# Kernel optimization log

Hardware: AMD Instinct MI355X
Metric: run time of the kernel (lower is better)

## Reference

```python
import jax, jax.numpy as jnp
import numpy as np

EPS_GEN = 1e-7   # GENConv message epsilon
LN_EPS = 1e-5    # torch LayerNorm default eps


def _ln(x, g, b):
    mu = x.mean(-1, keepdims=True)
    v = ((x - mu) ** 2).mean(-1, keepdims=True)
    return (x - mu) / jnp.sqrt(v + LN_EPS) * g + b


def _genconv(x, src, dst, N, t, W1, b1, g1, be1, W2, b2):
    # GENConv(aggr='softmax', learn_t, num_layers=2, norm='layer'), no edge_attr
    msg = jax.nn.relu(x[src]) + EPS_GEN                 # [E,H] gather + eps
    z = msg * t
    m = jax.ops.segment_max(z, dst, num_segments=N)      # scatter-max [N,H]
    e = jnp.exp(z - m[dst])
    denom = jax.ops.segment_sum(e, dst, num_segments=N) + 1e-16
    alpha = e / denom[dst]                               # per-neighborhood softmax
    out = jax.ops.segment_sum(msg * alpha, dst, num_segments=N) + x  # aggregate + root
    h = jax.nn.relu(_ln(out @ W1 + b1, g1, be1))         # MLP [H,2H] + LN + ReLU
    return h @ W2 + b2                                   # [2H,H] plain last layer


def setup_inputs():
    key = jax.random.key(0)
    ks = jax.random.split(key, 24)
    N, E, Fin, H = 100000, 1600000, 16, 64
    s = 0.02
    d = {
        'x': jax.random.normal(ks[0], (N, Fin), jnp.float32),
        'edge_index': jax.random.randint(ks[1], (2, E), 0, N, dtype=jnp.int32),
        'W_enc': jax.random.normal(ks[2], (Fin, H), jnp.float32) * s,
        'b_enc': jnp.zeros((H,), jnp.float32),
        't1': jnp.float32(1.0),
        'W1a': jax.random.normal(ks[3], (H, 2 * H), jnp.float32) * s,
        'b1a': jnp.zeros((2 * H,), jnp.float32),
        'g1a': jnp.ones((2 * H,), jnp.float32),
        'be1a': jnp.zeros((2 * H,), jnp.float32),
        'W1b': jax.random.normal(ks[4], (2 * H, H), jnp.float32) * s,
        'b1b': jnp.zeros((H,), jnp.float32),
        'g_n1': jnp.ones((H,), jnp.float32),
        'b_n1': jnp.zeros((H,), jnp.float32),
        't2': jnp.float32(1.0),
        'W2a': jax.random.normal(ks[5], (H, 2 * H), jnp.float32) * s,
        'b2a': jnp.zeros((2 * H,), jnp.float32),
        'g2a': jnp.ones((2 * H,), jnp.float32),
        'be2a': jnp.zeros((2 * H,), jnp.float32),
        'W2b': jax.random.normal(ks[6], (2 * H, H), jnp.float32) * s,
        'b2b': jnp.zeros((H,), jnp.float32),
        'g_n0': jnp.ones((H,), jnp.float32),
        'b_n0': jnp.zeros((H,), jnp.float32),
        'W_lin': jax.random.normal(ks[7], (H, 1), jnp.float32) * s,
        'b_lin': jnp.zeros((1,), jnp.float32),
    }
    return d


def reference(x, edge_index, W_enc, b_enc, t1, W1a, b1a, g1a, be1a, W1b, b1b,
              g_n1, b_n1, t2, W2a, b2a, g2a, be2a, W2b, b2b, g_n0, b_n0,
              W_lin, b_lin):
    N = x.shape[0]
    src, dst = edge_index[0], edge_index[1]
    h = x @ W_enc + b_enc                                   # node encoder
    h = _genconv(h, src, dst, N, t1, W1a, b1a, g1a, be1a, W1b, b1b)  # layers[0].conv (bare)
    # layers[1]: DeepGCNLayer res+ -> x + conv(act(norm(x)))  (dropout = identity, deterministic ref)
    r = _genconv(jax.nn.relu(_ln(h, g_n1, b_n1)), src, dst, N, t2,
                 W2a, b2a, g2a, be2a, W2b, b2b)
    h = h + r
    h = jax.nn.relu(_ln(h, g_n0, b_n0))                     # layers[0].norm / act at the end
    logits = h @ W_lin + b_lin                              # [N,1]
    return jax.nn.sigmoid(logits), logits
```

## Files before the change

kernel.cpp:

```cpp
#include <hip/hip_runtime.h>
#include <math.h>

constexpr int HD   = 64;
constexpr int HD2  = 128;
constexpr int SCAP = 48;
constexpr int NPW  = 4;
constexpr int NPB  = 16;
constexpr int PSH  = 14;
constexpr int EPB  = 2048;

constexpr int SO = 68;
constexpr int SU = 132;
constexpr int SY = 68;

constexpr float FXS  = 8192.f;
constexpr float FXSI = 1.f / 8192.f;

typedef short  bf16x8 __attribute__((ext_vector_type(8)));
typedef float  f32x4  __attribute__((ext_vector_type(4)));

__device__ __forceinline__ unsigned short fix16(float v) {
    int q = (int)(fmaxf(v, 0.f) * FXS + 0.5f);
    return (unsigned short)min(q, 65535);
}

__device__ __forceinline__ float wave_sum(float v) {
#pragma unroll
    for (int off = 32; off > 0; off >>= 1) v += __shfl_xor(v, off, 64);
    return v;
}

__device__ __forceinline__ void splitf(float f, short& hi, short& lo) {
    unsigned u = __float_as_uint(f);
    hi = (short)(u >> 16);
    float lf = f - __uint_as_float(u & 0xffff0000u);
    lo = (short)(__float_as_uint(lf) >> 16);
}

__device__ __forceinline__ void split8(const float* p, bf16x8& hi, bf16x8& lo) {
    float v[8];
    *(float4*)&v[0] = *(const float4*)p;
    *(float4*)&v[4] = *(const float4*)(p + 4);
#pragma unroll
    for (int j = 0; j < 8; j++) { short h, l; splitf(v[j], h, l); hi[j] = h; lo[j] = l; }
}

__global__ void prep_kernel(const int* __restrict__ ei,
                            int* __restrict__ cursor, int* __restrict__ slots,
                            const float* __restrict__ x,
                            const float* __restrict__ W,
                            const float* __restrict__ b,
                            float* __restrict__ h,
                            unsigned short* __restrict__ g,
                            const float* __restrict__ L1W1, const float* __restrict__ L1W2,
                            const float* __restrict__ L2W1, const float* __restrict__ L2W2,
                            short* __restrict__ swz,
                            int E, int N, int SB, int encB) {
    if (blockIdx.x < (unsigned)SB) {
        int p = blockIdx.x & 7;
        int base = (blockIdx.x >> 3) * EPB;
        for (int off = threadIdx.x; off < EPB; off += 256) {
            int e = base + off;
            if (e < E) {
                int dst = ei[E + e];
                if ((dst >> PSH) == p) {
                    int src = ei[e];
                    int pos = atomicAdd(&cursor[dst], 1);
                    if (pos < SCAP) slots[(unsigned)(dst * SCAP + pos)] = src;
                }
            }
        }
    } else if (blockIdx.x < (unsigned)(SB + encB)) {
        int i = (blockIdx.x - SB) * 256 + threadIdx.x;
        if (i >= N * HD) return;
        int n = i >> 6, j = i & 63;
        const float* xr = x + (unsigned)(n * 16);
        float acc = b[j];
#pragma unroll
        for (int k = 0; k < 16; k++) acc += xr[k] * W[k * HD + j];
        h[i] = acc;
        g[i] = fix16(acc);
    } else {
        int sb = blockIdx.x - SB - encB;
        int layer = sb >> 3;
        int idx = (sb & 7) * 256 + threadIdx.x;
        const float* Wa = layer ? L2W1 : L1W1;
        const float* Wb = layer ? L2W2 : L1W2;
        short* base = swz + layer * 32768;
        if (idx < 1024) {
            int ks = idx >> 9, rem = idx & 511;
            int nt = rem >> 6, lane = rem & 63;
#pragma unroll
            for (int j = 0; j < 8; j++) {
                int k = ks * 32 + (lane >> 4) * 8 + j;
                int n = nt * 16 + (lane & 15);
                short hh, ll; splitf(Wa[k * HD2 + n], hh, ll);
                base[idx * 8 + j] = hh; base[8192 + idx * 8 + j] = ll;
            }
        } else {
            int jdx = idx - 1024;
            int ks = jdx >> 8, rem = jdx & 255;
            int nt = rem >> 6, lane = rem & 63;
#pragma unroll
            for (int j = 0; j < 8; j++) {
                int k = ks * 32 + (lane >> 4) * 8 + j;
                int n = nt * 16 + (lane & 15);
                short hh, ll; splitf(Wb[k * HD + n], hh, ll);
                base[16384 + jdx * 8 + j] = hh; base[24576 + jdx * 8 + j] = ll;
            }
        }
    }
}

template <int MODE>
__global__ void __launch_bounds__(256) conv_kernel(
    const unsigned short* __restrict__ gin,
    const float* __restrict__ hroot,
    const int* __restrict__ deg_arr, const int* __restrict__ slots,
    const float* __restrict__ tptr,
    const short* __restrict__ W1hi, const short* __restrict__ W1lo,
    const float* __restrict__ b1,
    const float* __restrict__ g1, const float* __restrict__ be1,
    const short* __restrict__ W2hi, const short* __restrict__ W2lo,
    const float* __restrict__ b2,
    const float* __restrict__ gn, const float* __restrict__ bn,
    const float* __restrict__ resid,
    const float* __restrict__ wlin, const float* __restrict__ blin,
    float* __restrict__ outA, unsigned short* __restrict__ outG, int N) {
    __shared__ float s_out[NPB][SO];
    __shared__ float s_u[NPB][SU];
    __shared__ float s_y[NPB][SY];
    int wv = threadIdx.x >> 6, j = threadIdx.x & 63;
    int q = j >> 4;
    int c = (j & 15) << 2;
    int nb = blockIdx.x * NPB + wv * NPW;
    float t = tptr[0];

    int deg[NPW], sid[NPW];
#pragma unroll
    for (int u = 0; u < NPW; u++) {
        int n = nb + u;
        int d = (n < N) ? min(deg_arr[n], SCAP) : 0;
        deg[u] = d;
        sid[u] = (j < d) ? slots[(unsigned)(n * SCAP + j)] : 0;
    }
#pragma unroll
    for (int u = 0; u < NPW; u++) {
        int n = nb + u;
        int bl = wv * NPW + u;
        if (n < N) {
            int d = deg[u];
            float4 ae = {0.f, 0.f, 0.f, 0.f}, aw = {0.f, 0.f, 0.f, 0.f};
            for (int base = 0; base < d; base += 16) {
#pragma unroll
                for (int bb = 0; bb < 4; bb++) {
                    int i = base + bb * 4 + q;
                    int s = __shfl(sid[u], i, 64);
                    if (i < d) {
                        ushort4 uv = *(const ushort4*)(gin + (unsigned)((s << 6) | c));
                        float m0 = fmaf((float)uv.x, FXSI, 1e-7f);
                        float m1 = fmaf((float)uv.y, FXSI, 1e-7f);
                        float m2 = fmaf((float)uv.z, FXSI, 1e-7f);
                        float m3 = fmaf((float)uv.w, FXSI, 1e-7f);
                        float e0 = __expf(m0 * t), e1 = __expf(m1 * t);
                        float e2 = __expf(m2 * t), e3 = __expf(m3 * t);
                        ae.x += e0; ae.y += e1; ae.z += e2; ae.w += e3;
                        aw.x = fmaf(m0, e0, aw.x); aw.y = fmaf(m1, e1, aw.y);
                        aw.z = fmaf(m2, e2, aw.z); aw.w = fmaf(m3, e3, aw.w);
                    }
                }
            }
#pragma unroll
            for (int off = 16; off <= 32; off <<= 1) {
                ae.x += __shfl_xor(ae.x, off, 64); ae.y += __shfl_xor(ae.y, off, 64);
                ae.z += __shfl_xor(ae.z, off, 64); ae.w += __shfl_xor(ae.w, off, 64);
                aw.x += __shfl_xor(aw.x, off, 64); aw.y += __shfl_xor(aw.y, off, 64);
                aw.z += __shfl_xor(aw.z, off, 64); aw.w += __shfl_xor(aw.w, off, 64);
            }
            if (q == 0) {
                float4 o;
                if (MODE == 0) {
                    float4 hv = *(const float4*)(hroot + (unsigned)((n << 6) | c));
                    o.x = aw.x / (ae.x + 1e-16f) + hv.x;
                    o.y = aw.y / (ae.y + 1e-16f) + hv.y;
                    o.z = aw.z / (ae.z + 1e-16f) + hv.z;
                    o.w = aw.w / (ae.w + 1e-16f) + hv.w;
                } else {
                    ushort4 uv = *(const ushort4*)(gin + (unsigned)((n << 6) | c));
                    o.x = aw.x / (ae.x + 1e-16f) + (float)uv.x * FXSI;
                    o.y = aw.y / (ae.y + 1e-16f) + (float)uv.y * FXSI;
                    o.z = aw.z / (ae.z + 1e-16f) + (float)uv.z * FXSI;
                    o.w = aw.w / (ae.w + 1e-16f) + (float)uv.w * FXSI;
                }
                *(float4*)&s_out[bl][c] = o;
            }
        } else if (q == 0) {
            float4 z = {0.f, 0.f, 0.f, 0.f};
            *(float4*)&s_out[bl][c] = z;
        }
    }
    __syncthreads();

    int mrow = j & 15, kq = j >> 4, ncol = j & 15;
    {
        f32x4 acc[2];
#pragma unroll
        for (int i = 0; i < 2; i++) {
            float bb = b1[(wv * 2 + i) * 16 + ncol];
            acc[i] = (f32x4){bb, bb, bb, bb};
        }
#pragma unroll
        for (int ks = 0; ks < 2; ks++) {
            bf16x8 ah, al;
            split8(&s_out[mrow][ks * 32 + kq * 8], ah, al);
#pragma unroll
            for (int i = 0; i < 2; i++) {
                int nt = wv * 2 + i;
                int fo = (((ks * 8 + nt) * 64 + j) << 3);
                bf16x8 bh = *(const bf16x8*)(W1hi + fo);
                bf16x8 bl = *(const bf16x8*)(W1lo + fo);
                acc[i] = __builtin_amdgcn_mfma_f32_16x16x32_bf16(al, bh, acc[i], 0, 0, 0);
                acc[i] = __builtin_amdgcn_mfma_f32_16x16x32_bf16(ah, bl, acc[i], 0, 0, 0);
                acc[i] = __builtin_amdgcn_mfma_f32_16x16x32_bf16(ah, bh, acc[i], 0, 0, 0);
            }
        }
#pragma unroll
        for (int i = 0; i < 2; i++)
#pragma unroll
            for (int r = 0; r < 4; r++)
                s_u[kq * 4 + r][(wv * 2 + i) * 16 + ncol] = acc[i][r];
    }
    __syncthreads();

    {
        float g1a_ = g1[j], g1b_ = g1[HD + j];
        float be1a_ = be1[j], be1b_ = be1[HD + j];
#pragma unroll
        for (int u = 0; u < NPW; u++) {
            int bl = wv * NPW + u;
            float u0 = s_u[bl][j], u1 = s_u[bl][HD + j];
            float mu = wave_sum(u0 + u1) * (1.f / HD2);
            float d0 = u0 - mu, d1 = u1 - mu;
            float var = wave_sum(d0 * d0 + d1 * d1) * (1.f / HD2);
            float rstd = rsqrtf(var + 1e-5f);
            s_u[bl][j]      = fmaxf(d0 * rstd * g1a_ + be1a_, 0.f);
            s_u[bl][HD + j] = fmaxf(d1 * rstd * g1b_ + be1b_, 0.f);
        }
    }
    __syncthreads();

    {
        float bb = b2[wv * 16 + ncol];
        f32x4 acc = (f32x4){bb, bb, bb, bb};
#pragma unroll
        for (int ks = 0; ks < 4; ks++) {
            bf16x8 ah, al;
            split8(&s_u[mrow][ks * 32 + kq * 8], ah, al);
            int fo = (((ks * 4 + wv) * 64 + j) << 3);
            bf16x8 bh = *(const bf16x8*)(W2hi + fo);
            bf16x8 bl = *(const bf16x8*)(W2lo + fo);
            acc = __builtin_amdgcn_mfma_f32_16x16x32_bf16(al, bh, acc, 0, 0, 0);
            acc = __builtin_amdgcn_mfma_f32_16x16x32_bf16(ah, bl, acc, 0, 0, 0);
            acc = __builtin_amdgcn_mfma_f32_16x16x32_bf16(ah, bh, acc, 0, 0, 0);
        }
#pragma unroll
        for (int r = 0; r < 4; r++)
            s_y[kq * 4 + r][wv * 16 + ncol] = acc[r];
    }
    __syncthreads();

    float gn_ = gn[j], bn_ = bn[j];
    float wl = (MODE == 1) ? wlin[j] : 0.f;
#pragma unroll
    for (int u = 0; u < NPW; u++) {
        int n = nb + u;
        if (n >= N) continue;
        float yv = s_y[wv * NPW + u][j];
        unsigned oidx = (unsigned)((n << 6) | j);
        if (MODE == 0) {
            outA[oidx] = yv;
            float mu = wave_sum(yv) * (1.f / HD);
            float d = yv - mu;
            float var = wave_sum(d * d) * (1.f / HD);
            float rstd = rsqrtf(var + 1e-5f);
            outG[oidx] = fix16(d * rstd * gn_ + bn_);
        } else {
            float hf = yv + resid[oidx];
            float mu = wave_sum(hf) * (1.f / HD);
            float d = hf - mu;
            float var = wave_sum(d * d) * (1.f / HD);
            float rstd = rsqrtf(var + 1e-5f);
            float h2 = fmaxf(d * rstd * gn_ + bn_, 0.f);
            float dot = wave_sum(h2 * wl);
            if (j == 0) {
                float logit = dot + blin[0];
                outA[n] = 1.f / (1.f + __expf(-logit));
                outA[N + n] = logit;
            }
        }
    }
}

extern "C" void kernel_launch(void* const* d_in, const int* in_sizes, int n_in,
                              void* d_out, int out_size, void* d_ws, size_t ws_size,
                              hipStream_t stream) {
    const float* x     = (const float*)d_in[0];
    const int*   ei    = (const int*)  d_in[1];
    const float* W_enc = (const float*)d_in[2];
    const float* b_enc = (const float*)d_in[3];
    const float* t1    = (const float*)d_in[4];
    const float* W1a   = (const float*)d_in[5];
    const float* b1a   = (const float*)d_in[6];
    const float* g1a   = (const float*)d_in[7];
    const float* be1a  = (const float*)d_in[8];
    const float* W1b   = (const float*)d_in[9];
    const float* b1b   = (const float*)d_in[10];
    const float* g_n1  = (const float*)d_in[11];
    const float* b_n1  = (const float*)d_in[12];
    const float* t2    = (const float*)d_in[13];
    const float* W2a   = (const float*)d_in[14];
    const float* b2a   = (const float*)d_in[15];
    const float* g2a   = (const float*)d_in[16];
    const float* be2a  = (const float*)d_in[17];
    const float* W2b   = (const float*)d_in[18];
    const float* b2b   = (const float*)d_in[19];
    const float* g_n0  = (const float*)d_in[20];
    const float* b_n0  = (const float*)d_in[21];
    const float* W_lin = (const float*)d_in[22];
    const float* b_lin = (const float*)d_in[23];

    int N = in_sizes[0] / 16;
    int E = in_sizes[1] / 2;
    size_t NH = (size_t)N * HD;

    float* h0           = (float*)d_ws;
    float* h1           = h0 + NH;
    unsigned short* g0  = (unsigned short*)(h1 + NH);
    unsigned short* g1f = g0 + NH;
    int*   cursor       = (int*)(g1f + NH);
    int*   slots        = cursor + N;
    short* swz          = (short*)(slots + (size_t)N * SCAP);

    int nodeBlocks = (N + NPB - 1) / NPB;
    int chunks     = (E + EPB - 1) / EPB;
    int SB         = chunks * 8;
    int encBlocks  = (int)((NH + 255) / 256);

    hipMemsetAsync(cursor, 0, (size_t)N * sizeof(int), stream);

    prep_kernel<<<SB + encBlocks + 16, 256, 0, stream>>>(
        ei, cursor, slots, x, W_enc, b_enc, h0, g0,
        W1a, W1b, W2a, W2b, swz, E, N, SB, encBlocks);

    short* W1hi_1 = swz,          *W1lo_1 = swz + 8192;
    short* W2hi_1 = swz + 16384,  *W2lo_1 = swz + 24576;
    short* W1hi_2 = swz + 32768,  *W1lo_2 = swz + 40960;
    short* W2hi_2 = swz + 49152,  *W2lo_2 = swz + 57344;

    conv_kernel<0><<<nodeBlocks, 256, 0, stream>>>(
        g0, h0, cursor, slots, t1,
        W1hi_1, W1lo_1, b1a, g1a, be1a, W2hi_1, W2lo_1, b1b,
        g_n1, b_n1, nullptr, nullptr, nullptr, h1, g1f, N);

    conv_kernel<1><<<nodeBlocks, 256, 0, stream>>>(
        g1f, nullptr, cursor, slots, t2,
        W1hi_2, W1lo_2, b2a, g2a, be2a, W2hi_2, W2lo_2, b2b,
        g_n0, b_n0, h1, W_lin, b_lin, (float*)d_out, nullptr, N);
}
```

Measured before the change: 407.9 us.

## Precompute per-node exp weights in fp16 and pack with fixed-point messages

The producer of each layer's gather input now computes exp(m*t) once per node and packs it as fp16 next to the 16-bit fixed-point message in one 32-bit word. The gather loop then reads both instead of evaluating four exponentials per edge, and issues all four neighbour loads before consuming them. Root and residual features are stored as scaled int16 instead of fp32 to cut bandwidth. This doubles the bytes read per gathered neighbour and adds quantization error to the exp weights, root and residual, with clamping if values exceed the int16 range.

New measurement: 383.2 us. 1.06x faster.

```diff
diff --git a/kernel.cpp b/kernel.cpp
--- a/kernel.cpp
+++ b/kernel.cpp
@@ -1,4 +1,5 @@
 #include <hip/hip_runtime.h>
+#include <hip/hip_fp16.h>
 #include <math.h>
 
 constexpr int HD   = 64;
@@ -15,19 +16,39 @@
 
 constexpr float FXS  = 8192.f;
 constexpr float FXSI = 1.f / 8192.f;
+constexpr float RXS  = 16384.f;
+constexpr float RXSI = 1.f / 16384.f;
+constexpr float HXS  = 4096.f;
+constexpr float HXSI = 1.f / 4096.f;
 
 typedef short  bf16x8 __attribute__((ext_vector_type(8)));
 typedef float  f32x4  __attribute__((ext_vector_type(4)));
 
-__device__ __forceinline__ unsigned short fix16(float v) {
-    int q = (int)(fmaxf(v, 0.f) * FXS + 0.5f);
-    return (unsigned short)min(q, 65535);
-}
-
 __device__ __forceinline__ float wave_sum(float v) {
 #pragma unroll
     for (int off = 32; off > 0; off >>= 1) v += __shfl_xor(v, off, 64);
     return v;
+}
+
+__device__ __forceinline__ unsigned int packme(float v, float t) {
+    int q = (int)(fmaxf(v, 0.f) * FXS + 0.5f);
+    unsigned int mu = (unsigned int)min(q, 65535);
+    float m = fmaf((float)mu, FXSI, 1e-7f);
+    float e = __expf(m * t);
+    __half eh = __float2half(e);
+    unsigned short eu = *(unsigned short*)&eh;
+    return (mu << 16) | (unsigned int)eu;
+}
+
+__device__ __forceinline__ float h2f_lo(unsigned int w) {
+    unsigned short lo = (unsigned short)(w & 0xffffu);
+    __half h = *(__half*)&lo;
+    return __half2float(h);
+}
+
+__device__ __forceinline__ short f2s16(float v, float s) {
+    int q = (int)rintf(v * s);
+    return (short)max(-32768, min(32767, q));
 }
 
 __device__ __forceinline__ void splitf(float f, short& hi, short& lo) {
@@ -50,8 +71,9 @@
                             const float* __restrict__ x,
                             const float* __restrict__ W,
                             const float* __restrict__ b,
-                            float* __restrict__ h,
-                            unsigned short* __restrict__ g,
+                            const float* __restrict__ t1ptr,
+                            short* __restrict__ h0s,
+                            unsigned int* __restrict__ g,
                             const float* __restrict__ L1W1, const float* __restrict__ L1W2,
                             const float* __restrict__ L2W1, const float* __restrict__ L2W2,
                             short* __restrict__ swz,
@@ -74,12 +96,13 @@
         int i = (blockIdx.x - SB) * 256 + threadIdx.x;
         if (i >= N * HD) return;
         int n = i >> 6, j = i & 63;
+        float t1v = t1ptr[0];
         const float* xr = x + (unsigned)(n * 16);
         float acc = b[j];
 #pragma unroll
         for (int k = 0; k < 16; k++) acc += xr[k] * W[k * HD + j];
-        h[i] = acc;
-        g[i] = fix16(acc);
+        h0s[i] = f2s16(acc, RXS);
+        g[i] = packme(acc, t1v);
     } else {
         int sb = blockIdx.x - SB - encB;
         int layer = sb >> 3;
@@ -114,19 +137,20 @@
 
 template <int MODE>
 __global__ void __launch_bounds__(256) conv_kernel(
-    const unsigned short* __restrict__ gin,
-    const float* __restrict__ hroot,
+    const unsigned int* __restrict__ gin,
+    const short* __restrict__ hroot,
     const int* __restrict__ deg_arr, const int* __restrict__ slots,
-    const float* __restrict__ tptr,
+    const float* __restrict__ tnext,
     const short* __restrict__ W1hi, const short* __restrict__ W1lo,
     const float* __restrict__ b1,
     const float* __restrict__ g1, const float* __restrict__ be1,
     const short* __restrict__ W2hi, const short* __restrict__ W2lo,
     const float* __restrict__ b2,
     const float* __restrict__ gn, const float* __restrict__ bn,
-    const float* __restrict__ resid,
+    const short* __restrict__ resid,
     const float* __restrict__ wlin, const float* __restrict__ blin,
-    float* __restrict__ outA, unsigned short* __restrict__ outG, int N) {
+    float* __restrict__ outA, short* __restrict__ outH,
+    unsigned int* __restrict__ outG, int N) {
     __shared__ float s_out[NPB][SO];
     __shared__ float s_u[NPB][SU];
     __shared__ float s_y[NPB][SY];
@@ -134,7 +158,7 @@
     int q = j >> 4;
     int c = (j & 15) << 2;
     int nb = blockIdx.x * NPB + wv * NPW;
-    float t = tptr[0];
+    float tn = (MODE == 0) ? tnext[0] : 0.f;
 
     int deg[NPW], sid[NPW];
 #pragma unroll
@@ -152,18 +176,22 @@
             int d = deg[u];
             float4 ae = {0.f, 0.f, 0.f, 0.f}, aw = {0.f, 0.f, 0.f, 0.f};
             for (int base = 0; base < d; base += 16) {
+                uint4 uv[4];
 #pragma unroll
                 for (int bb = 0; bb < 4; bb++) {
                     int i = base + bb * 4 + q;
                     int s = __shfl(sid[u], i, 64);
+                    uv[bb] = *(const uint4*)(gin + (unsigned)((s << 6) | c));
+                }
+#pragma unroll
+                for (int bb = 0; bb < 4; bb++) {
+                    int i = base + bb * 4 + q;
                     if (i < d) {
-                        ushort4 uv = *(const ushort4*)(gin + (unsigned)((s << 6) | c));
-                        float m0 = fmaf((float)uv.x, FXSI, 1e-7f);
-                        float m1 = fmaf((float)uv.y, FXSI, 1e-7f);
-                        float m2 = fmaf((float)uv.z, FXSI, 1e-7f);
-                        float m3 = fmaf((float)uv.w, FXSI, 1e-7f);
-                        float e0 = __expf(m0 * t), e1 = __expf(m1 * t);
-                        float e2 = __expf(m2 * t), e3 = __expf(m3 * t);
+                        uint4 w = uv[bb];
+                        float m0 = (float)(w.x >> 16), e0 = h2f_lo(w.x);
+                        float m1 = (float)(w.y >> 16), e1 = h2f_lo(w.y);
+                        float m2 = (float)(w.z >> 16), e2 = h2f_lo(w.z);
+                        float m3 = (float)(w.w >> 16), e3 = h2f_lo(w.w);
                         ae.x += e0; ae.y += e1; ae.z += e2; ae.w += e3;
                         aw.x = fmaf(m0, e0, aw.x); aw.y = fmaf(m1, e1, aw.y);
                         aw.z = fmaf(m2, e2, aw.z); aw.w = fmaf(m3, e3, aw.w);
@@ -179,18 +207,22 @@
             }
             if (q == 0) {
                 float4 o;
+                float n0 = fmaf(ae.x, 1e-7f, aw.x * FXSI);
+                float n1 = fmaf(ae.y, 1e-7f, aw.y * FXSI);
+                float n2 = fmaf(ae.z, 1e-7f, aw.z * FXSI);
+                float n3 = fmaf(ae.w, 1e-7f, aw.w * FXSI);
                 if (MODE == 0) {
-                    float4 hv = *(const float4*)(hroot + (unsigned)((n << 6) | c));
-                    o.x = aw.x / (ae.x + 1e-16f) + hv.x;
-                    o.y = aw.y / (ae.y + 1e-16f) + hv.y;
-                    o.z = aw.z / (ae.z + 1e-16f) + hv.z;
-                    o.w = aw.w / (ae.w + 1e-16f) + hv.w;
+                    short4 hv = *(const short4*)(hroot + (unsigned)((n << 6) | c));
+                    o.x = n0 / (ae.x + 1e-16f) + (float)hv.x * RXSI;
+                    o.y = n1 / (ae.y + 1e-16f) + (float)hv.y * RXSI;
+                    o.z = n2 / (ae.z + 1e-16f) + (float)hv.z * RXSI;
+                    o.w = n3 / (ae.w + 1e-16f) + (float)hv.w * RXSI;
                 } else {
-                    ushort4 uv = *(const ushort4*)(gin + (unsigned)((n << 6) | c));
-                    o.x = aw.x / (ae.x + 1e-16f) + (float)uv.x * FXSI;
-                    o.y = aw.y / (ae.y + 1e-16f) + (float)uv.y * FXSI;
-                    o.z = aw.z / (ae.z + 1e-16f) + (float)uv.z * FXSI;
-                    o.w = aw.w / (ae.w + 1e-16f) + (float)uv.w * FXSI;
+                    uint4 w = *(const uint4*)(gin + (unsigned)((n << 6) | c));
+                    o.x = n0 / (ae.x + 1e-16f) + (float)(w.x >> 16) * FXSI;
+                    o.y = n1 / (ae.y + 1e-16f) + (float)(w.y >> 16) * FXSI;
+                    o.z = n2 / (ae.z + 1e-16f) + (float)(w.z >> 16) * FXSI;
+                    o.w = n3 / (ae.w + 1e-16f) + (float)(w.w >> 16) * FXSI;
                 }
                 *(float4*)&s_out[bl][c] = o;
             }
@@ -278,14 +310,14 @@
         float yv = s_y[wv * NPW + u][j];
         unsigned oidx = (unsigned)((n << 6) | j);
         if (MODE == 0) {
-            outA[oidx] = yv;
+            outH[oidx] = f2s16(yv, HXS);
             float mu = wave_sum(yv) * (1.f / HD);
             float d = yv - mu;
             float var = wave_sum(d * d) * (1.f / HD);
             float rstd = rsqrtf(var + 1e-5f);
-            outG[oidx] = fix16(d * rstd * gn_ + bn_);
+            outG[oidx] = packme(d * rstd * gn_ + bn_, tn);
         } else {
-            float hf = yv + resid[oidx];
+            float hf = yv + (float)resid[oidx] * HXSI;
             float mu = wave_sum(hf) * (1.f / HD);
             float d = hf - mu;
             float var = wave_sum(d * d) * (1.f / HD);
@@ -333,10 +365,10 @@
     int E = in_sizes[1] / 2;
     size_t NH = (size_t)N * HD;
 
-    float* h0           = (float*)d_ws;
-    float* h1           = h0 + NH;
-    unsigned short* g0  = (unsigned short*)(h1 + NH);
-    unsigned short* g1f = g0 + NH;
+    short* h0s          = (short*)d_ws;
+    short* h1s          = h0s + NH;
+    unsigned int* g0    = (unsigned int*)(h1s + NH);
+    unsigned int* g1f   = g0 + NH;
     int*   cursor       = (int*)(g1f + NH);
     int*   slots        = cursor + N;
     short* swz          = (short*)(slots + (size_t)N * SCAP);
@@ -349,7 +381,7 @@
     hipMemsetAsync(cursor, 0, (size_t)N * sizeof(int), stream);
 
     prep_kernel<<<SB + encBlocks + 16, 256, 0, stream>>>(
-        ei, cursor, slots, x, W_enc, b_enc, h0, g0,
+        ei, cursor, slots, x, W_enc, b_enc, t1, h0s, g0,
         W1a, W1b, W2a, W2b, swz, E, N, SB, encBlocks);
 
     short* W1hi_1 = swz,          *W1lo_1 = swz + 8192;
@@ -358,12 +390,14 @@
     short* W2hi_2 = swz + 49152,  *W2lo_2 = swz + 57344;
 
     conv_kernel<0><<<nodeBlocks, 256, 0, stream>>>(
-        g0, h0, cursor, slots, t1,
+        g0, h0s, cursor, slots, t2,
         W1hi_1, W1lo_1, b1a, g1a, be1a, W2hi_1, W2lo_1, b1b,
-        g_n1, b_n1, nullptr, nullptr, nullptr, h1, g1f, N);
+        g_n1, b_n1, nullptr, nullptr, nullptr,
+        nullptr, h1s, g1f, N);
 
     conv_kernel<1><<<nodeBlocks, 256, 0, stream>>>(
         g1f, nullptr, cursor, slots, t2,
         W1hi_2, W1lo_2, b2a, g2a, be2a, W2hi_2, W2lo_2, b2b,
-        g_n0, b_n0, h1, W_lin, b_lin, (float*)d_out, nullptr, N);
-}
+        g_n0, b_n0, h1s, W_lin, b_lin,
+        (float*)d_out, nullptr, nullptr, N);
+}
```
